# Kernel optimization log

Measured on AMD Instinct MI355X. Metric: run time of the kernel, lower is better.

## Reference

```python
import jax, jax.numpy as jnp
import numpy as np
import math

B, C, H, T, S = 2, 1024, 16, 2048, 2048
DH = C // H  # 64


def setup_inputs() -> dict:
    key = jax.random.key(0)
    ks = jax.random.split(key, 10)
    target = jax.random.normal(ks[0], (B, C, T), dtype=jnp.float32)
    source = jax.random.normal(ks[1], (B, C, S), dtype=jnp.float32)
    target_mask = (jax.random.uniform(ks[2], (B, 1, T)) < 0.9).astype(jnp.float32)
    source_mask = (jax.random.uniform(ks[3], (B, 1, S)) < 0.9).astype(jnp.float32)
    scale = 1.0 / math.sqrt(C)
    Wq = jax.random.normal(ks[4], (C, C), dtype=jnp.float32) * scale
    bq = jnp.zeros((C,), dtype=jnp.float32)
    Wk = jax.random.normal(ks[5], (C, C), dtype=jnp.float32) * scale
    bk = jnp.zeros((C,), dtype=jnp.float32)
    Wv = jax.random.normal(ks[6], (C, C), dtype=jnp.float32) * scale
    bv = jnp.zeros((C,), dtype=jnp.float32)
    return {"target": target, "source": source, "target_mask": target_mask,
            "source_mask": source_mask, "Wq": Wq, "bq": bq, "Wk": Wk, "bk": bk,
            "Wv": Wv, "bv": bv}


def _proj(W, b, x):
    # 1x1 Conv1d == pointwise channel mixing: [B,C,L] -> [B,C,L]
    return jnp.einsum('oc,bcl->bol', W, x) + b[None, :, None]


def reference(target, source, target_mask, source_mask, Wq, bq, Wk, bk, Wv, bv):
    q = _proj(Wq, bq, target).reshape(B, H, DH, T)
    k = _proj(Wk, bk, source).reshape(B, H, DH, S)
    v = _proj(Wv, bv, source).reshape(B, H, DH, S)
    # dot: [B,H,T,S], scaled by sqrt(d_head) (key.size(2) in torch)
    dot = jnp.einsum('bhdt,bhds->bhts', q, k) / math.sqrt(DH)
    # available mask [B,1,T,S], broadcast over heads
    avail = jnp.einsum('bjt,bjs->bjts', target_mask, source_mask)
    dot = avail * dot - (1.0 - avail) * 1.0e6
    # NOTE: original torch code overwrites the masked amap with a plain
    # softmax of the (masked) dot; we reproduce that exactly.
    amap = jax.nn.softmax(dot, axis=-1)
    out = jnp.einsum('bhts,bhds->bhdt', amap, v)  # [B,H,DH,T]
    return out.reshape(B, C, T)
```

## Files before the change

kernel.cpp:

```cpp
#include <hip/hip_runtime.h>

#define BB 2
#define CC 1024
#define HH 16
#define TT 2048
#define SS 2048
#define LL 2048
#define C2MASK 1442695.0f
#define NT_TILES (SS / 64)

typedef unsigned short u16;
typedef unsigned int u32;
typedef __attribute__((ext_vector_type(8))) short short8;
typedef __attribute__((ext_vector_type(4))) float f32x4;
typedef __attribute__((ext_vector_type(4))) unsigned short us4;
typedef __attribute__((ext_vector_type(2))) unsigned int u32x2;
typedef __attribute__((ext_vector_type(4))) unsigned int u32x4;

__device__ __forceinline__ u16 f2bf(float f) {
    union { float f; unsigned int i; } x; x.f = f;
    unsigned int r = x.i + 0x7FFFu + ((x.i >> 16) & 1u);
    return (u16)(r >> 16);
}
__device__ __forceinline__ float exp2_hw(float x) {
    float r;
    asm("v_exp_f32 %0, %1" : "=v"(r) : "v"(x));
    return r;
}
__device__ __forceinline__ float max3f(float a, float b, float c) {
    float r;
    asm("v_max3_f32 %0, %1, %2, %3" : "=v"(r) : "v"(a), "v"(b), "v"(c));
    return r;
}
__device__ __forceinline__ u32 cvtpk_bf16(float lo, float hi) {
    u32 r;
    asm("v_cvt_pk_bf16_f32 %0, %1, %2" : "=v"(r) : "v"(lo), "v"(hi));
    return r;
}
__device__ __forceinline__ void gload_lds16(const u16* g, u16* l) {
    __builtin_amdgcn_global_load_lds(
        (const __attribute__((address_space(1))) unsigned int*)g,
        (__attribute__((address_space(3))) unsigned int*)l, 16, 0, 0);
}

__global__ __launch_bounds__(256) void prep(
    const float* __restrict__ target, const float* __restrict__ source,
    const float* __restrict__ smaskp,
    const float* __restrict__ Wq, const float* __restrict__ Wk, const float* __restrict__ Wv,
    u16* __restrict__ Wb, u16* __restrict__ Tt, u16* __restrict__ St,
    float* __restrict__ sbias, float* __restrict__ zrow)
{
    __shared__ float xs[64][65];
    const int tid = threadIdx.x;
    const int bid = blockIdx.x;

    if (bid < 2048) {
        const int img  = bid >> 9;
        const int tile = bid & 511;
        const int ct = tile >> 5, lt = tile & 31;
        const int c0 = ct * 64, l0 = lt * 64;
        const float* src = ((img < 2) ? target : source) + (size_t)(img & 1) * CC * LL;
        u16* dst = ((img < 2) ? Tt : St) + (size_t)(img & 1) * LL * CC;

        const int i = tid >> 2, seg = (tid & 3) * 16;
        const float* g = src + (size_t)(c0 + i) * LL + l0 + seg;
        f32x4 a0 = *(const f32x4*)g;
        f32x4 a1 = *(const f32x4*)(g + 4);
        f32x4 a2 = *(const f32x4*)(g + 8);
        f32x4 a3 = *(const f32x4*)(g + 12);
#pragma unroll
        for (int j = 0; j < 4; j++) {
            xs[i][seg + j]      = a0[j];
            xs[i][seg + 4 + j]  = a1[j];
            xs[i][seg + 8 + j]  = a2[j];
            xs[i][seg + 12 + j] = a3[j];
        }
        __syncthreads();

        const int l = tid >> 2, cseg = (tid & 3) * 16;
        float f[16];
#pragma unroll
        for (int j = 0; j < 16; j++) f[j] = xs[cseg + j][l];
        u32x4 o0, o1;
#pragma unroll
        for (int k = 0; k < 4; k++) {
            o0[k] = cvtpk_bf16(f[2 * k], f[2 * k + 1]);
            o1[k] = cvtpk_bf16(f[8 + 2 * k], f[9 + 2 * k]);
        }
        u16* d = dst + (size_t)(l0 + l) * CC + c0 + cseg;
        *(u32x4*)d = o0;
        *(u32x4*)(d + 8) = o1;
    } else {
        const int wblk = bid - 2048;
        const size_t idx = (size_t)wblk * 2048 + tid * 8;
        const int m = (int)(idx >> 20);
        const size_t rem = idx & 1048575;
        const float* srcp = ((m == 0) ? Wq : (m == 1) ? Wk : Wv) + rem;
        f32x4 a = *(const f32x4*)srcp;
        f32x4 c = *(const f32x4*)(srcp + 4);
        u32x4 o;
        o[0] = cvtpk_bf16(a[0], a[1]); o[1] = cvtpk_bf16(a[2], a[3]);
        o[2] = cvtpk_bf16(c[0], c[1]); o[3] = cvtpk_bf16(c[2], c[3]);
        *(u32x4*)(Wb + ((size_t)m << 20) + rem) = o;

        if (wblk < 2) {
            const int b = wblk;
            const float* sm = smaskp + (size_t)b * SS;
            float* sb = sbias + (size_t)b * SS;
            for (int s = tid; s < SS; s += 256) {
                sb[s] = (sm[s] > 0.5f) ? 0.0f : -C2MASK;
                if (b == 0) zrow[s] = 0.0f;
            }
        }
    }
}

__global__ __launch_bounds__(256) void qkv_gemm(
    const u16* __restrict__ Wb, const u16* __restrict__ Tt, const u16* __restrict__ St,
    const float* __restrict__ bq, const float* __restrict__ bk, const float* __restrict__ bv,
    const float* __restrict__ tmaskp,
    u16* __restrict__ Qb, u16* __restrict__ Kb, u16* __restrict__ Vb)
{
    __shared__ __align__(16) u16 As[128 * 64];
    __shared__ __align__(16) u16 Bs[128 * 64];

    const int p = blockIdx.z >> 1;
    const int b = blockIdx.z & 1;
    const int m0 = blockIdx.y * 128;
    const int n0 = blockIdx.x * 128;

    const u16* A  = Wb + ((size_t)p << 20) + (size_t)m0 * CC;
    const u16* Bx = ((p == 0) ? Tt : St) + (size_t)b * LL * CC + (size_t)n0 * CC;
    const float* bias = (p == 0) ? bq : (p == 1) ? bk : bv;

    const int tid  = threadIdx.x;
    const int lane = tid & 63;
    const int wid  = tid >> 6;
    const int ln   = lane & 15;
    const int q    = lane >> 4;
    const int wm   = (wid >> 1) * 64;
    const int wn   = (wid & 1) * 64;

    const int r0 = tid >> 3;
    const int cs = (tid & 7) ^ (r0 & 7);
    const u16* ag = A  + (size_t)r0 * CC + cs * 8;
    const u16* bg = Bx + (size_t)r0 * CC + cs * 8;
    const int lb = wid * 512;

    f32x4 acc[4][4];
#pragma unroll
    for (int i = 0; i < 4; i++)
#pragma unroll
        for (int j = 0; j < 4; j++) acc[i][j] = (f32x4){0.f, 0.f, 0.f, 0.f};

    const int sx0 = ((q ^ (ln & 7)) << 3);
    const int sx1 = (((q + 4) ^ (ln & 7)) << 3);

    for (int k0 = 0; k0 < CC; k0 += 64) {
        __syncthreads();
#pragma unroll
        for (int i = 0; i < 4; i++) {
            gload_lds16(ag + (size_t)i * 32 * CC + k0, &As[lb + i * 2048]);
            gload_lds16(bg + (size_t)i * 32 * CC + k0, &Bs[lb + i * 2048]);
        }
        __syncthreads();

        short8 aF[4][2], bF[4][2];
#pragma unroll
        for (int mt = 0; mt < 4; mt++) {
            const u16* ar = As + (wm + mt * 16 + ln) * 64;
            aF[mt][0] = *(const short8*)(ar + sx0);
            aF[mt][1] = *(const short8*)(ar + sx1);
        }
#pragma unroll
        for (int nt = 0; nt < 4; nt++) {
            const u16* br = Bs + (wn + nt * 16 + ln) * 64;
            bF[nt][0] = *(const short8*)(br + sx0);
            bF[nt][1] = *(const short8*)(br + sx1);
        }
#pragma unroll
        for (int mt = 0; mt < 4; mt++)
#pragma unroll
            for (int nt = 0; nt < 4; nt++) {
                acc[mt][nt] = __builtin_amdgcn_mfma_f32_16x16x32_bf16(aF[mt][0], bF[nt][0], acc[mt][nt], 0, 0, 0);
                acc[mt][nt] = __builtin_amdgcn_mfma_f32_16x16x32_bf16(aF[mt][1], bF[nt][1], acc[mt][nt], 0, 0, 0);
            }
    }

    const float oscale = (p == 0) ? 0.18033688011112042f : 1.0f;
#pragma unroll
    for (int mt = 0; mt < 4; mt++) {
        const int o_base = m0 + wm + mt * 16 + q * 4;
        float bsf[4];
#pragma unroll
        for (int r = 0; r < 4; r++) bsf[r] = bias[o_base + r];
#pragma unroll
        for (int nt = 0; nt < 4; nt++) {
            const int l = n0 + wn + nt * 16 + ln;
            if (p == 2) {
#pragma unroll
                for (int r = 0; r < 4; r++)
                    Vb[((size_t)b * CC + o_base + r) * SS + l] = f2bf(acc[mt][nt][r] + bsf[r]);
            } else {
                const int h = o_base >> 6;
                const int d = o_base & 63;
                u16* dst = (p == 0) ? Qb : Kb;
                float sc2 = oscale;
                if (p == 0) sc2 = oscale * tmaskp[(size_t)b * TT + l];
                us4 pk;
#pragma unroll
                for (int r = 0; r < 4; r++) pk[r] = (u16)f2bf((acc[mt][nt][r] + bsf[r]) * sc2);
                *(us4*)(dst + ((size_t)(b * HH + h) * TT + l) * 64 + d) = pk;
            }
        }
    }
}

__global__ __launch_bounds__(256, 4) void attn_k(
    const u16* __restrict__ Qb, const u16* __restrict__ Kb, const u16* __restrict__ Vb,
    const float* __restrict__ tmask, const float* __restrict__ sbias,
    const float* __restrict__ zrow, float* __restrict__ out)
{
    __shared__ __align__(16) u16 Ks[2][64 * 64];
    __shared__ __align__(16) u16 Vs[2][64 * 64];
    __shared__ __align__(16) u16 Ps[4][16 * 64];

    const int tid  = threadIdx.x;
    const int wid  = tid >> 6;
    const int lane = tid & 63;
    const int ln   = lane & 15;
    const int q    = lane >> 4;

    const int idx   = blockIdx.x;
    const int xcd   = idx & 7;
    const int rest  = idx >> 3;
    const int ttile = rest & 31;
    const int bh    = (rest >> 5) * 8 + xcd;
    const int b     = bh >> 4;
    const int h     = bh & 15;
    const int t0    = ttile * 64 + wid * 16;

    const u16* Qp = Qb + (size_t)bh * TT * 64;
    const u16* Kp = Kb + (size_t)bh * SS * 64;
    const u16* Vp = Vb + ((size_t)b * CC + h * 64) * SS;

    const float tm = tmask[(size_t)b * TT + t0 + ln];
    const float* bp = (tm > 0.5f) ? (sbias + (size_t)b * SS) : zrow;

    const int r0  = tid >> 3;
    const int c0  = tid & 7;
    const int cs0 = c0 ^ (r0 & 7);
    const u16* kg0 = Kp + (size_t)r0 * 64 + cs0 * 8;
    const u16* kg1 = Kp + (size_t)(r0 + 32) * 64 + cs0 * 8;
    const u16* vg0 = Vp + (size_t)r0 * SS + cs0 * 8;
    const u16* vg1 = Vp + (size_t)(r0 + 32) * SS + cs0 * 8;
    const int lw0 = wid * 512;
    const int lw1 = 2048 + wid * 512;

#define STAGE(buf, sn) do {                                         \
        gload_lds16(kg0 + (size_t)(sn) * 64, &Ks[buf][lw0]);        \
        gload_lds16(kg1 + (size_t)(sn) * 64, &Ks[buf][lw1]);        \
        gload_lds16(vg0 + (sn), &Vs[buf][lw0]);                     \
        gload_lds16(vg1 + (sn), &Vs[buf][lw1]);                     \
    } while (0)

    short8 qB0 = *(const short8*)(Qp + (size_t)(t0 + ln) * 64 + q * 8);
    short8 qB1 = *(const short8*)(Qp + (size_t)(t0 + ln) * 64 + 32 + q * 8);

    float mR = -3.0e38f, lR = 0.f;
    f32x4 oA[4];
#pragma unroll
    for (int dt = 0; dt < 4; dt++) oA[dt] = (f32x4){0.f, 0.f, 0.f, 0.f};

    const int sx0 = ((q ^ (ln & 7)) << 3);
    const int sx1 = (((q + 4) ^ (ln & 7)) << 3);

    u16* pw = Ps[wid];

    STAGE(0, 0);

    int cur = 0;
#pragma unroll 2
    for (int it = 0; it < NT_TILES; ++it) {
        const int s0 = it * 64;
        __syncthreads();
        if (it + 1 < NT_TILES) STAGE(cur ^ 1, s0 + 64);

        const u16* KsB = Ks[cur];
        const u16* VsB = Vs[cur];

        f32x4 sc[4];
#pragma unroll
        for (int nt = 0; nt < 4; nt++) {
            const u16* kr = KsB + (nt * 16 + ln) * 64;
            short8 k0 = *(const short8*)(kr + sx0);
            short8 k1 = *(const short8*)(kr + sx1);
            f32x4 bias = *(const f32x4*)(bp + s0 + nt * 16 + q * 4);
            sc[nt] = __builtin_amdgcn_mfma_f32_16x16x32_bf16(k0, qB0, bias, 0, 0, 0);
            sc[nt] = __builtin_amdgcn_mfma_f32_16x16x32_bf16(k1, qB1, sc[nt], 0, 0, 0);
        }

        float m4[4];
#pragma unroll
        for (int nt = 0; nt < 4; nt++)
            m4[nt] = fmaxf(max3f(sc[nt][0], sc[nt][1], sc[nt][2]), sc[nt][3]);
        float m_ = fmaxf(max3f(m4[0], m4[1], m4[2]), m4[3]);
        m_ = fmaxf(m_, __shfl_xor(m_, 16, 64));
        m_ = fmaxf(m_, __shfl_xor(m_, 32, 64));

        if (!__all(m_ - mR <= 8.0f)) {
            const float mN = fmaxf(mR, m_);
            const float al = exp2_hw(mR - mN);
            lR *= al;
#pragma unroll
            for (int dt = 0; dt < 4; dt++) oA[dt] *= al;
            mR = mN;
        }

        float s4[4];
#pragma unroll
        for (int nt = 0; nt < 4; nt++) {
#pragma unroll
            for (int r = 0; r < 4; r++) sc[nt][r] = exp2_hw(sc[nt][r] - mR);
            s4[nt] = (sc[nt][0] + sc[nt][1]) + (sc[nt][2] + sc[nt][3]);
        }
        float s_ = (s4[0] + s4[1]) + (s4[2] + s4[3]);
        s_ += __shfl_xor(s_, 16, 64);
        s_ += __shfl_xor(s_, 32, 64);
        lR += s_;

#pragma unroll
        for (int nt = 0; nt < 4; nt++) {
            u32x2 w;
            w[0] = cvtpk_bf16(sc[nt][0], sc[nt][1]);
            w[1] = cvtpk_bf16(sc[nt][2], sc[nt][3]);
            const int chunk = (nt << 1) | (q >> 1);
            *(u32x2*)(pw + ln * 64 + ((chunk ^ (ln & 7)) << 3) + ((q & 1) << 2)) = w;
        }
        short8 pB0 = *(const short8*)(pw + ln * 64 + sx0);
        short8 pB1 = *(const short8*)(pw + ln * 64 + sx1);
#pragma unroll
        for (int dt = 0; dt < 4; dt++) {
            const u16* vr = VsB + (dt * 16 + ln) * 64;
            short8 v0 = *(const short8*)(vr + sx0);
            short8 v1 = *(const short8*)(vr + sx1);
            oA[dt] = __builtin_amdgcn_mfma_f32_16x16x32_bf16(v0, pB0, oA[dt], 0, 0, 0);
            oA[dt] = __builtin_amdgcn_mfma_f32_16x16x32_bf16(v1, pB1, oA[dt], 0, 0, 0);
        }
        cur ^= 1;
    }
#undef STAGE

    const float inv = 1.0f / lR;
#pragma unroll
    for (int dt = 0; dt < 4; dt++)
#pragma unroll
        for (int r = 0; r < 4; r++)
            out[((size_t)b * CC + h * 64 + dt * 16 + q * 4 + r) * TT + t0 + ln] =
                oA[dt][r] * inv;
}

extern "C" void kernel_launch(void* const* d_in, const int* in_sizes, int n_in,
                              void* d_out, int out_size, void* d_ws, size_t ws_size,
                              hipStream_t stream)
{
    const float* target = (const float*)d_in[0];
    const float* source = (const float*)d_in[1];
    const float* tmask  = (const float*)d_in[2];
    const float* smask  = (const float*)d_in[3];
    const float* Wq = (const float*)d_in[4];
    const float* bq = (const float*)d_in[5];
    const float* Wk = (const float*)d_in[6];
    const float* bk = (const float*)d_in[7];
    const float* Wv = (const float*)d_in[8];
    const float* bv = (const float*)d_in[9];

    u16* ws = (u16*)d_ws;
    const size_t N1 = (size_t)BB * CC * TT;
    u16* Qb = ws;
    u16* Kb = ws + N1;
    u16* Vb = ws + 2 * N1;
    float* sbias = (float*)(ws + 3 * N1);
    float* zrow  = sbias + 2 * SS;
    u16* Wb = (u16*)(zrow + SS);
    u16* Tt = Wb + 3u * 1048576u;
    u16* St = Tt + (size_t)BB * LL * CC;

    prep<<<dim3(3584, 1, 1), dim3(256, 1, 1), 0, stream>>>(
        target, source, smask, Wq, Wk, Wv, Wb, Tt, St, sbias, zrow);
    qkv_gemm<<<dim3(TT/128, CC/128, 6), dim3(256, 1, 1), 0, stream>>>(
        Wb, Tt, St, bq, bk, bv, tmask, Qb, Kb, Vb);
    attn_k<<<dim3(BB*HH*(TT/64), 1, 1), dim3(256, 1, 1), 0, stream>>>(
        Qb, Kb, Vb, tmask, sbias, zrow, (float*)d_out);
}
```

Baseline: 205.3 us.

## Double-buffer QKV GEMM K-loop with BK=32 and add MFMA priority hints in attention

```diff
diff --git a/kernel.cpp b/kernel.cpp
--- a/kernel.cpp
+++ b/kernel.cpp
@@ -121,8 +121,8 @@
     const float* __restrict__ tmaskp,
     u16* __restrict__ Qb, u16* __restrict__ Kb, u16* __restrict__ Vb)
 {
-    __shared__ __align__(16) u16 As[128 * 64];
-    __shared__ __align__(16) u16 Bs[128 * 64];
+    __shared__ __align__(16) u16 As[2][4096];
+    __shared__ __align__(16) u16 Bs[2][4096];
 
     const int p = blockIdx.z >> 1;
     const int b = blockIdx.z & 1;
@@ -141,51 +141,54 @@
     const int wm   = (wid >> 1) * 64;
     const int wn   = (wid & 1) * 64;
 
-    const int r0 = tid >> 3;
-    const int cs = (tid & 7) ^ (r0 & 7);
-    const u16* ag = A  + (size_t)r0 * CC + cs * 8;
-    const u16* bg = Bx + (size_t)r0 * CC + cs * 8;
+    int row1, c1, row2, c2;
+    { const int s = tid;       const int pp = s >> 3, j = s & 7, i = j ^ (pp & 7);
+      row1 = 2 * pp + (i >> 2); c1 = i & 3; }
+    { const int s = tid + 256; const int pp = s >> 3, j = s & 7, i = j ^ (pp & 7);
+      row2 = 2 * pp + (i >> 2); c2 = i & 3; }
+    const u16* ag1 = A  + (size_t)row1 * CC + c1 * 8;
+    const u16* ag2 = A  + (size_t)row2 * CC + c2 * 8;
+    const u16* bg1 = Bx + (size_t)row1 * CC + c1 * 8;
+    const u16* bg2 = Bx + (size_t)row2 * CC + c2 * 8;
     const int lb = wid * 512;
 
+#define QSTAGE(buf, k0) do {                                  \
+        gload_lds16(ag1 + (k0), &As[buf][lb]);                \
+        gload_lds16(ag2 + (k0), &As[buf][2048 + lb]);         \
+        gload_lds16(bg1 + (k0), &Bs[buf][lb]);                \
+        gload_lds16(bg2 + (k0), &Bs[buf][2048 + lb]);         \
+    } while (0)
+
     f32x4 acc[4][4];
 #pragma unroll
     for (int i = 0; i < 4; i++)
 #pragma unroll
         for (int j = 0; j < 4; j++) acc[i][j] = (f32x4){0.f, 0.f, 0.f, 0.f};
 
-    const int sx0 = ((q ^ (ln & 7)) << 3);
-    const int sx1 = (((q + 4) ^ (ln & 7)) << 3);
-
-    for (int k0 = 0; k0 < CC; k0 += 64) {
+    const int loff = (ln >> 1) * 64 + (((((ln & 1) << 2) | q)) ^ (ln >> 1)) * 8;
+
+    QSTAGE(0, 0);
+
+    int cur = 0;
+    for (int k0 = 0; k0 < CC; k0 += 32) {
         __syncthreads();
-#pragma unroll
-        for (int i = 0; i < 4; i++) {
-            gload_lds16(ag + (size_t)i * 32 * CC + k0, &As[lb + i * 2048]);
-            gload_lds16(bg + (size_t)i * 32 * CC + k0, &Bs[lb + i * 2048]);
-        }
-        __syncthreads();
-
-        short8 aF[4][2], bF[4][2];
-#pragma unroll
-        for (int mt = 0; mt < 4; mt++) {
-            const u16* ar = As + (wm + mt * 16 + ln) * 64;
-            aF[mt][0] = *(const short8*)(ar + sx0);
-            aF[mt][1] = *(const short8*)(ar + sx1);
-        }
-#pragma unroll
-        for (int nt = 0; nt < 4; nt++) {
-            const u16* br = Bs + (wn + nt * 16 + ln) * 64;
-            bF[nt][0] = *(const short8*)(br + sx0);
-            bF[nt][1] = *(const short8*)(br + sx1);
-        }
+        if (k0 + 32 < CC) QSTAGE(cur ^ 1, k0 + 32);
+
+        short8 aF[4], bF[4];
 #pragma unroll
         for (int mt = 0; mt < 4; mt++)
-#pragma unroll
-            for (int nt = 0; nt < 4; nt++) {
-                acc[mt][nt] = __builtin_amdgcn_mfma_f32_16x16x32_bf16(aF[mt][0], bF[nt][0], acc[mt][nt], 0, 0, 0);
-                acc[mt][nt] = __builtin_amdgcn_mfma_f32_16x16x32_bf16(aF[mt][1], bF[nt][1], acc[mt][nt], 0, 0, 0);
-            }
+            aF[mt] = *(const short8*)(&As[cur][wm * 32 + mt * 512 + loff]);
+#pragma unroll
+        for (int nt = 0; nt < 4; nt++)
+            bF[nt] = *(const short8*)(&Bs[cur][wn * 32 + nt * 512 + loff]);
+#pragma unroll
+        for (int mt = 0; mt < 4; mt++)
+#pragma unroll
+            for (int nt = 0; nt < 4; nt++)
+                acc[mt][nt] = __builtin_amdgcn_mfma_f32_16x16x32_bf16(aF[mt], bF[nt], acc[mt][nt], 0, 0, 0);
+        cur ^= 1;
     }
+#undef QSTAGE
 
     const float oscale = (p == 0) ? 0.18033688011112042f : 1.0f;
 #pragma unroll
@@ -290,6 +293,7 @@
         const u16* VsB = Vs[cur];
 
         f32x4 sc[4];
+        __builtin_amdgcn_s_setprio(1);
 #pragma unroll
         for (int nt = 0; nt < 4; nt++) {
             const u16* kr = KsB + (nt * 16 + ln) * 64;
@@ -299,6 +303,7 @@
             sc[nt] = __builtin_amdgcn_mfma_f32_16x16x32_bf16(k0, qB0, bias, 0, 0, 0);
             sc[nt] = __builtin_amdgcn_mfma_f32_16x16x32_bf16(k1, qB1, sc[nt], 0, 0, 0);
         }
+        __builtin_amdgcn_s_setprio(0);
 
         float m4[4];
 #pragma unroll
@@ -339,6 +344,7 @@
         }
         short8 pB0 = *(const short8*)(pw + ln * 64 + sx0);
         short8 pB1 = *(const short8*)(pw + ln * 64 + sx1);
+        __builtin_amdgcn_s_setprio(1);
 #pragma unroll
         for (int dt = 0; dt < 4; dt++) {
             const u16* vr = VsB + (dt * 16 + ln) * 64;
@@ -347,6 +353,7 @@
             oA[dt] = __builtin_amdgcn_mfma_f32_16x16x32_bf16(v0, pB0, oA[dt], 0, 0, 0);
             oA[dt] = __builtin_amdgcn_mfma_f32_16x16x32_bf16(v1, pB1, oA[dt], 0, 0, 0);
         }
+        __builtin_amdgcn_s_setprio(0);
         cur ^= 1;
     }
 #undef STAGE
```

New measurement: 200.3 us. 1.03x faster.
